# Optimization experiments

Hardware: AMD Instinct MI355X
Metric: run time of the kernel (lower is better)

The kernel has to match this reference:

```python
import jax, jax.numpy as jnp
import numpy as np

N_NODES = 100000
N_EDGES = 1600000
ATOM_EMB = 64
BOND_EMB = 16
MSG_DIM = 64
OUT_HIDDEN = 128
N_MOLS = 2048
MSG_PASSES = 4


def setup_inputs() -> dict:
    key = jax.random.key(0)
    ks = jax.random.split(key, 16)
    x = jax.random.randint(ks[0], (N_NODES,), 0, 119)
    edge_attr = jax.random.randint(ks[1], (N_EDGES,), 0, 4)
    edge_index = jax.random.randint(ks[2], (2, N_EDGES), 0, N_NODES)
    batch = jnp.sort(jax.random.randint(ks[3], (N_NODES,), 0, N_MOLS))
    s = 0.02
    atom_table = jax.random.normal(ks[4], (119, ATOM_EMB), jnp.float32) * s
    bond_table = jax.random.normal(ks[5], (4, BOND_EMB), jnp.float32) * s
    Wi = jax.random.normal(ks[6], (ATOM_EMB + BOND_EMB, MSG_DIM), jnp.float32) * s
    bi = jnp.zeros((MSG_DIM,), jnp.float32)
    Wu = jax.random.normal(ks[7], (ATOM_EMB + BOND_EMB + MSG_DIM, MSG_DIM), jnp.float32) * s
    bu = jnp.zeros((MSG_DIM,), jnp.float32)
    W1 = jax.random.normal(ks[8], (MSG_DIM, OUT_HIDDEN), jnp.float32) * s
    b1 = jnp.zeros((OUT_HIDDEN,), jnp.float32)
    W2 = jax.random.normal(ks[9], (OUT_HIDDEN, 1), jnp.float32) * s
    b2 = jnp.zeros((1,), jnp.float32)
    return {"x": x, "edge_attr": edge_attr, "edge_index": edge_index, "batch": batch,
            "atom_table": atom_table, "bond_table": bond_table,
            "Wi": Wi, "bi": bi, "Wu": Wu, "bu": bu,
            "W1": W1, "b1": b1, "W2": W2, "b2": b2}


def reference(x, edge_attr, edge_index, batch, atom_table, bond_table, Wi, bi, Wu, bu, W1, b1, W2, b2):
    atom = atom_table[x]                      # [N, ATOM_EMB]
    bond = bond_table[edge_attr]              # [E, BOND_EMB]
    src, dst = edge_index[0], edge_index[1]
    atom_src = atom[src]                      # [E, ATOM_EMB]
    ab = jnp.concatenate([atom_src, bond], axis=1)
    msg = jax.nn.relu(ab @ Wi + bi)           # [E, MSG_DIM]
    for _ in range(MSG_PASSES):
        agg = jax.ops.segment_sum(msg, dst, num_segments=N_NODES)  # [N, MSG_DIM]
        upd_in = jnp.concatenate([ab, agg[src]], axis=1)           # [E, 144]
        msg = jax.nn.relu(upd_in @ Wu + bu)
    node_state = jax.ops.segment_sum(msg, dst, num_segments=N_NODES)
    mol_state = jax.ops.segment_sum(node_state, batch, num_segments=N_MOLS)
    h = jax.nn.relu(mol_state @ W1 + b1)
    return (h @ W2 + b2).squeeze(-1)          # [N_MOLS]
```

## Files before the change

### kernel.cpp

```cpp
#include <hip/hip_runtime.h>

#define MSG 64
#define SLICE_SHIFT 9
#define SLICE_N (1 << SLICE_SHIFT)
#define MAXSLICES 256
#define REP 8
#define CAP_R 1536
#define CAP_E 12288
#define CAP_B 16384
#define NBIN 64

typedef _Float16 h2 __attribute__((ext_vector_type(2)));
typedef _Float16 h4 __attribute__((ext_vector_type(4)));
typedef _Float16 h8 __attribute__((ext_vector_type(8)));

__device__ inline h8 relu8(h8 v) {
    h8 z = {};
    return __builtin_elementwise_max(v, z);
}

__device__ inline h2 u2h(unsigned u) { union { unsigned u; h2 h; } c; c.u = u; return c.h; }

__global__ void setup_kernel(const float* __restrict__ atom, const float* __restrict__ bond,
                             const float* __restrict__ Wi, const float* __restrict__ bi,
                             const float* __restrict__ Wu, const float* __restrict__ bu,
                             const float* __restrict__ Wagg,
                             _Float16* __restrict__ tAi, _Float16* __restrict__ tBi,
                             _Float16* __restrict__ tAu, _Float16* __restrict__ tBu,
                             unsigned* __restrict__ wst, int* __restrict__ gcur,
                             int* __restrict__ bcnt, float* __restrict__ mol,
                             int AR, int K, int ab) {
    int b = blockIdx.x;
    if (b < 2 * ab + 2) {
        bool upd = b >= ab + 1;
        const float* W = upd ? Wu : Wi;
        int lb = upd ? b - (ab + 1) : b;
        if (lb < ab) {
            _Float16* tA = upd ? tAu : tAi;
            int t = lb * 256 + threadIdx.x;
            if (t < AR * MSG) {
                int i = t & 63, a = t >> 6;
                float s = 0.f;
                for (int k = 0; k < 64; ++k) s = fmaf(atom[a * 64 + k], W[k * 64 + i], s);
                tA[t] = (_Float16)s;
            }
        } else {
            _Float16* tBo = upd ? tBu : tBi;
            const float* bias = upd ? bu : bi;
            const float* W16 = W + 64 * MSG;
            int t = threadIdx.x;
            int i = t & 63, r = t >> 6;
            float s = bias[i];
            for (int k = 0; k < 16; ++k) s = fmaf(bond[r * 16 + k], W16[k * 64 + i], s);
            tBo[t] = (_Float16)s;
        }
    } else if (b < 2 * ab + 10) {
        int t = (b - (2 * ab + 2)) * 256 + threadIdx.x;
        if (t < 2048) {
            int k2 = t >> 6, c = t & 63;
            h2 h; h[0] = (_Float16)Wagg[(2 * k2) * 64 + c]; h[1] = (_Float16)Wagg[(2 * k2 + 1) * 64 + c];
            union { h2 h; unsigned u; } cv; cv.h = h;
            wst[k2 * 64 + c] = cv.u;
        }
    } else if (b == 2 * ab + 10) {
        for (int q = threadIdx.x; q < K * REP; q += 256) gcur[q] = q * CAP_R;
        if (threadIdx.x < NBIN) bcnt[threadIdx.x] = 0;
    } else {
        int t = (b - (2 * ab + 11)) * 256 + threadIdx.x;
        ((float4*)mol)[t] = make_float4(0.f, 0.f, 0.f, 0.f);
    }
}

__global__ __launch_bounds__(256) void partition_kernel(
    const int* __restrict__ ei, const int* __restrict__ eattr,
    int E, int* __restrict__ gcur, unsigned long long* __restrict__ aux, int K)
{
    __shared__ int cnt[MAXSLICES];
    __shared__ int lexcl[MAXSLICES];
    __shared__ int gbase[MAXSLICES];
    __shared__ int wsum[4];
    __shared__ unsigned long long stage[1024];
    if (threadIdx.x < MAXSLICES) cnt[threadIdx.x] = 0;
    __syncthreads();
    int rep = blockIdx.x & (REP - 1);
    int e0 = blockIdx.x * 1024;
    int total = min(1024, E - e0);
    int sl[4]; int rk[4]; unsigned long long rec[4];
#pragma unroll
    for (int r = 0; r < 4; ++r) {
        sl[r] = -1;
        int e = e0 + r * 256 + threadIdx.x;
        if (e < E) {
            int s = ei[e], d = ei[E + e];
            rec[r] = ((unsigned long long)((unsigned)s | ((unsigned)eattr[e] << 17)) << 17) | (unsigned)d;
            sl[r] = d >> SLICE_SHIFT;
            rk[r] = atomicAdd(&cnt[sl[r]], 1);
        }
    }
    __syncthreads();
    {
        int c = cnt[threadIdx.x];
        int lane = threadIdx.x & 63, w = threadIdx.x >> 6;
        int sc = c;
        for (int off = 1; off < 64; off <<= 1) { int t = __shfl_up(sc, off); if (lane >= off) sc += t; }
        if (lane == 63) wsum[w] = sc;
        __syncthreads();
        int add = 0;
        for (int q = 0; q < 3; ++q) if (w > q) add += wsum[q];
        lexcl[threadIdx.x] = sc + add - c;
        if (threadIdx.x < K && c > 0)
            gbase[threadIdx.x] = atomicAdd(&gcur[threadIdx.x * REP + rep], c);
    }
    __syncthreads();
#pragma unroll
    for (int r = 0; r < 4; ++r)
        if (sl[r] >= 0) stage[lexcl[sl[r]] + rk[r]] = rec[r];
    __syncthreads();
#pragma unroll
    for (int r = 0; r < 4; ++r) {
        int i = r * 256 + threadIdx.x;
        if (i < total) {
            unsigned long long a = stage[i];
            int s = (int)((unsigned)a & 0x1FFFFu) >> SLICE_SHIFT;
            aux[gbase[s] + (i - lexcl[s])] = a;
        }
    }
}

__global__ __launch_bounds__(1024) void place_kernel(
    const unsigned long long* __restrict__ aux, const int* __restrict__ gcur,
    int* __restrict__ nstart, int* __restrict__ bcnt, int* __restrict__ bucket,
    unsigned* __restrict__ packed, int N)
{
    __shared__ int cnt[SLICE_N];
    __shared__ int wsum[8];
    __shared__ unsigned stage[CAP_E];
    __shared__ int bc[NBIN];
    __shared__ int bb[NBIN];
    int s = blockIdx.x;
    int lo = s << SLICE_SHIFT;
    if (threadIdx.x < SLICE_N) cnt[threadIdx.x] = 0;
    if (threadIdx.x >= SLICE_N && threadIdx.x < SLICE_N + NBIN) bc[threadIdx.x - SLICE_N] = 0;
    __syncthreads();
    for (int r = 0; r < REP; ++r) {
        int q = s * REP + r;
        int start = q * CAP_R, end = gcur[q];
        for (int idx = start + threadIdx.x; idx < end; idx += 1024)
            atomicAdd(&cnt[(int)(aux[idx] & 0x1FFFFu) & (SLICE_N - 1)], 1);
    }
    __syncthreads();
    int c = 0, sc = 0;
    if (threadIdx.x < SLICE_N) {
        c = cnt[threadIdx.x];
        int lane = threadIdx.x & 63, w = threadIdx.x >> 6;
        sc = c;
        for (int off = 1; off < 64; off <<= 1) { int t = __shfl_up(sc, off); if (lane >= off) sc += t; }
        if (lane == 63) wsum[w] = sc;
    }
    __syncthreads();
    int v = lo + threadIdx.x;
    int bin = -1, rk = 0;
    if (threadIdx.x < SLICE_N) {
        int w = threadIdx.x >> 6;
        int add = 0;
        for (int q = 0; q < 7; ++q) if (w > q) add += wsum[q];
        sc += add;
        if (v < N) {
            nstart[v] = s * CAP_E + sc - c;
            bin = min(c, NBIN - 1);
            rk = atomicAdd(&bc[bin], 1);
        }
    }
    __syncthreads();
    if (threadIdx.x < NBIN && bc[threadIdx.x] > 0)
        bb[threadIdx.x] = atomicAdd(&bcnt[threadIdx.x], bc[threadIdx.x]);
    __syncthreads();
    if (bin >= 0) bucket[bin * CAP_B + bb[bin] + rk] = v | (c << 17);
    if (threadIdx.x < SLICE_N) cnt[threadIdx.x] = sc - c;
    __syncthreads();
    for (int r = 0; r < REP; ++r) {
        int q = s * REP + r;
        int start = q * CAP_R, end = gcur[q];
        for (int idx = start + threadIdx.x; idx < end; idx += 1024) {
            unsigned long long a = aux[idx];
            int d = (int)(a & 0x1FFFFu);
            int p = atomicAdd(&cnt[d & (SLICE_N - 1)], 1);
            stage[p] = (unsigned)(a >> 17);
        }
    }
    __syncthreads();
    int totale = cnt[SLICE_N - 1];
    for (int i = threadIdx.x; i < totale; i += 1024)
        packed[s * CAP_E + i] = stage[i];
}

__global__ void compact_kernel(const int* __restrict__ bucket, const int* __restrict__ bcnt,
                               const int* __restrict__ nstart, int2* __restrict__ srt) {
    __shared__ int sbase;
    int b = blockIdx.x;
    if (threadIdx.x == 0) {
        int run = 0;
        for (int i = b + 1; i < NBIN; ++i) run += bcnt[i];
        sbase = run;
    }
    __syncthreads();
    int n = bcnt[b], base = sbase;
    for (int i = threadIdx.x; i < n; i += 256) {
        int e = bucket[b * CAP_B + i];
        int v = e & 0x1FFFF;
        srt[base + i] = make_int2(nstart[v], e);
    }
}

template <int MODE>
__global__ __launch_bounds__(256, 8) void gather_kernel(
    const unsigned* __restrict__ packed, const int2* __restrict__ srt,
    const _Float16* __restrict__ nodearr, const _Float16* __restrict__ tB,
    const unsigned* __restrict__ wst_g, const _Float16* __restrict__ tAu,
    const int* __restrict__ x, const _Float16* __restrict__ tAi,
    _Float16* __restrict__ out, int N)
{
    __shared__ _Float16 tbs[4 * 64];
    __shared__ unsigned wst[32 * 64];
    __shared__ _Float16 rowb[32][72];
    tbs[threadIdx.x] = tB[threadIdx.x];
    if (MODE != 2)
        for (int idx = threadIdx.x; idx < 2048; idx += 256) wst[idx] = wst_g[idx];
    __syncthreads();
    int t = blockIdx.x * 256 + threadIdx.x;
    int vi = t >> 3;
    int j = threadIdx.x & 7;
    int w = threadIdx.x >> 3;
    const h8* na8 = (const h8*)nodearr;
    const h8* tAi8 = (const h8*)tAi;
    const _Float16* tbsj = tbs + j * 8;
    auto ldrow = [&](unsigned q) -> h8 {
        if (MODE == 0) return tAi8[(long long)x[q & 0x1FFFFu] * 8 + j];
        else           return na8[(q & 0x1FFFFu) * 8 + j];
    };
    auto ldtb = [&](unsigned q) -> h8 { return *(const h8*)&tbsj[(q >> 17) * 64]; };
    h8 acc = {};
    int v = 0;
    bool valid = vi < N;
    if (valid) {
        int2 s2 = srt[vi];
        int e = s2.x;
        v = (int)((unsigned)s2.y & 0x1FFFFu);
        int end = e + (int)((unsigned)s2.y >> 17);
        for (; e + 7 < end; e += 8) {
            unsigned q0 = packed[e],     q1 = packed[e + 1], q2 = packed[e + 2], q3 = packed[e + 3];
            unsigned q4 = packed[e + 4], q5 = packed[e + 5], q6 = packed[e + 6], q7 = packed[e + 7];
            h8 m0 = ldrow(q0), m1 = ldrow(q1), m2 = ldrow(q2), m3 = ldrow(q3);
            h8 m4 = ldrow(q4), m5 = ldrow(q5), m6 = ldrow(q6), m7 = ldrow(q7);
            h8 s0 = relu8(m0 + ldtb(q0)), s1 = relu8(m1 + ldtb(q1));
            h8 s2v = relu8(m2 + ldtb(q2)), s3 = relu8(m3 + ldtb(q3));
            h8 s4 = relu8(m4 + ldtb(q4)), s5 = relu8(m5 + ldtb(q5));
            h8 s6 = relu8(m6 + ldtb(q6)), s7 = relu8(m7 + ldtb(q7));
            acc += ((s0 + s1) + (s2v + s3)) + ((s4 + s5) + (s6 + s7));
        }
        for (; e < end; ++e) {
            unsigned q0 = packed[e];
            acc += relu8(ldrow(q0) + ldtb(q0));
        }
    }
    if (MODE == 2) {
        if (valid) ((h8*)out)[(long long)v * 8 + j] = acc;
        return;
    }
    *(h8*)&rowb[w][j * 8] = acc;
    __syncthreads();
    if (!valid) return;
    const h2* rp = (const h2*)&rowb[w][0];
    const unsigned* wj = wst + j * 8;
    float o0 = 0.f, o1 = 0.f, o2 = 0.f, o3 = 0.f, o4 = 0.f, o5 = 0.f, o6 = 0.f, o7 = 0.f;
#pragma unroll
    for (int k2 = 0; k2 < 32; ++k2) {
        h2 r = rp[k2];
        uint4 wa = *(const uint4*)&wj[k2 * 64];
        uint4 wb = *(const uint4*)&wj[k2 * 64 + 4];
        o0 = __builtin_amdgcn_fdot2(r, u2h(wa.x), o0, false);
        o1 = __builtin_amdgcn_fdot2(r, u2h(wa.y), o1, false);
        o2 = __builtin_amdgcn_fdot2(r, u2h(wa.z), o2, false);
        o3 = __builtin_amdgcn_fdot2(r, u2h(wa.w), o3, false);
        o4 = __builtin_amdgcn_fdot2(r, u2h(wb.x), o4, false);
        o5 = __builtin_amdgcn_fdot2(r, u2h(wb.y), o5, false);
        o6 = __builtin_amdgcn_fdot2(r, u2h(wb.z), o6, false);
        o7 = __builtin_amdgcn_fdot2(r, u2h(wb.w), o7, false);
    }
    h8 ta = ((const h8*)tAu)[x[v] * 8 + j];
    h8 o;
    o[0] = (_Float16)(o0 + (float)ta[0]); o[1] = (_Float16)(o1 + (float)ta[1]);
    o[2] = (_Float16)(o2 + (float)ta[2]); o[3] = (_Float16)(o3 + (float)ta[3]);
    o[4] = (_Float16)(o4 + (float)ta[4]); o[5] = (_Float16)(o5 + (float)ta[5]);
    o[6] = (_Float16)(o6 + (float)ta[6]); o[7] = (_Float16)(o7 + (float)ta[7]);
    ((h8*)out)[(long long)v * 8 + j] = o;
}

__global__ void mol_pool_kernel(const _Float16* __restrict__ ns, const int* __restrict__ batch,
                                float* __restrict__ mol, int N) {
    int g = (blockIdx.x * blockDim.x + threadIdx.x) >> 4;
    int j = threadIdx.x & 15;
    int n0 = g * 32;
    if (n0 >= N) return;
    int n1 = min(n0 + 32, N);
    const h4* ns4 = (const h4*)ns;
    int cur = batch[n0];
    float ax = 0.f, ay = 0.f, az = 0.f, aw = 0.f;
    for (int n = n0; n < n1; ++n) {
        int b = batch[n];
        if (b != cur) {
            float* mp = &mol[(long long)cur * 64 + j * 4];
            atomicAdd(mp + 0, ax); atomicAdd(mp + 1, ay);
            atomicAdd(mp + 2, az); atomicAdd(mp + 3, aw);
            ax = ay = az = aw = 0.f; cur = b;
        }
        h4 vv = ns4[(long long)n * 16 + j];
        ax += (float)vv.x; ay += (float)vv.y; az += (float)vv.z; aw += (float)vv.w;
    }
    float* mp = &mol[(long long)cur * 64 + j * 4];
    atomicAdd(mp + 0, ax); atomicAdd(mp + 1, ay);
    atomicAdd(mp + 2, az); atomicAdd(mp + 3, aw);
}

__global__ void head_kernel(const float* __restrict__ mol, const float* __restrict__ W1,
                            const float* __restrict__ b1, const float* __restrict__ W2,
                            const float* __restrict__ b2, float* __restrict__ out) {
    int g = blockIdx.x;
    int j = threadIdx.x;
    float s = b1[j];
#pragma unroll
    for (int k = 0; k < 64; ++k) s = fmaf(mol[g * 64 + k], W1[k * 128 + j], s);
    s = fmaxf(s, 0.0f) * W2[j];
    __shared__ float red[128];
    red[j] = s;
    __syncthreads();
    for (int off = 64; off > 0; off >>= 1) {
        if (j < off) red[j] += red[j + off];
        __syncthreads();
    }
    if (j == 0) out[g] = red[0] + b2[0];
}

extern "C" void kernel_launch(void* const* d_in, const int* in_sizes, int n_in,
                              void* d_out, int out_size, void* d_ws, size_t ws_size,
                              hipStream_t stream) {
    const int*   x          = (const int*)d_in[0];
    const int*   eattr      = (const int*)d_in[1];
    const int*   ei         = (const int*)d_in[2];
    const int*   batch      = (const int*)d_in[3];
    const float* atom_table = (const float*)d_in[4];
    const float* bond_table = (const float*)d_in[5];
    const float* Wi         = (const float*)d_in[6];
    const float* bi         = (const float*)d_in[7];
    const float* Wu         = (const float*)d_in[8];
    const float* bu         = (const float*)d_in[9];
    const float* W1         = (const float*)d_in[10];
    const float* b1         = (const float*)d_in[11];
    const float* W2         = (const float*)d_in[12];
    const float* b2         = (const float*)d_in[13];

    const int N = in_sizes[0];
    const int E = in_sizes[1];
    const int M = out_size;
    const int AR = in_sizes[4] / 64;
    const int K = (N + SLICE_N - 1) >> SLICE_SHIFT;
    const int ab = (AR * MSG + 255) / 256;

    char* ws = (char*)d_ws;
    size_t off_b = 0;
    auto alloc = [&](size_t bytes) -> void* {
        void* p = ws + off_b;
        off_b = (off_b + bytes + 255) & ~(size_t)255;
        return p;
    };
    size_t nbytes = (size_t)N * MSG * 2;
    size_t abytes = (size_t)K * REP * CAP_R * 8;
    _Float16* bufA  = (_Float16*)alloc(nbytes);
    _Float16* bufB  = (_Float16*)alloc(nbytes > abytes ? nbytes : abytes);
    unsigned long long* aux = (unsigned long long*)bufB;
    unsigned* packed = (unsigned*)alloc((size_t)K * CAP_E * 4);
    int*      nstart = (int*)alloc((size_t)N * 4);
    int2*     srt    = (int2*)alloc((size_t)N * 8);
    int*      bucket = (int*)alloc((size_t)NBIN * CAP_B * 4);
    int*      bcnt   = (int*)alloc((size_t)NBIN * 4);
    int*      gcur   = (int*)alloc((size_t)K * REP * 4);
    _Float16* tAi    = (_Float16*)alloc((size_t)AR * MSG * 2);
    _Float16* tBi    = (_Float16*)alloc((size_t)4 * MSG * 2);
    _Float16* tAu    = (_Float16*)alloc((size_t)AR * MSG * 2);
    _Float16* tBu    = (_Float16*)alloc((size_t)4 * MSG * 2);
    unsigned* wstb   = (unsigned*)alloc((size_t)32 * 64 * 4);
    float*    mol    = (float*)alloc((size_t)M * MSG * 4);
    (void)ws_size; (void)n_in;

    const float* Wagg = Wu + 80 * MSG;

    setup_kernel<<<2 * ab + 11 + 128, 256, 0, stream>>>(atom_table, bond_table, Wi, bi, Wu, bu, Wagg,
                                                        tAi, tBi, tAu, tBu, wstb, gcur, bcnt, mol,
                                                        AR, K, ab);

    partition_kernel<<<(E + 1023) / 1024, 256, 0, stream>>>(ei, eattr, E, gcur, aux, K);
    place_kernel<<<K, 1024, 0, stream>>>(aux, gcur, nstart, bcnt, bucket, packed, N);
    compact_kernel<<<NBIN, 256, 0, stream>>>(bucket, bcnt, nstart, srt);

    const int gblocks = (int)(((long long)N * 8 + 255) / 256);
    gather_kernel<0><<<gblocks, 256, 0, stream>>>(packed, srt, nullptr, tBi, wstb, tAu, x, tAi, bufA, N);
    gather_kernel<1><<<gblocks, 256, 0, stream>>>(packed, srt, bufA, tBu, wstb, tAu, x, nullptr, bufB, N);
    gather_kernel<1><<<gblocks, 256, 0, stream>>>(packed, srt, bufB, tBu, wstb, tAu, x, nullptr, bufA, N);
    gather_kernel<1><<<gblocks, 256, 0, stream>>>(packed, srt, bufA, tBu, wstb, tAu, x, nullptr, bufB, N);
    gather_kernel<2><<<gblocks, 256, 0, stream>>>(packed, srt, bufB, tBu, nullptr, nullptr, nullptr, nullptr, bufA, N);

    mol_pool_kernel<<<(((N + 31) / 32) * 16 + 255) / 256, 256, 0, stream>>>(bufA, batch, mol, N);
    head_kernel<<<M, 128, 0, stream>>>(mol, W1, b1, W2, b2, (float*)d_out);
}
```

Baseline: 261.6 us.

## Pack partition records to 32 bits and fuse molecule pooling into head

Edge records in the partition stage now pack the source, bond type and low destination bits into 32 bits, with the slice id kept only in shared staging. This halves aux buffer traffic. Molecule pooling is folded into the head kernel: per-molecule node ranges come from a binary search over the sorted batch array in setup. This removes the atomic pooling kernel, the mol buffer zeroing and a launch. It relies on batch being sorted and on node ids fitting in 17 bits.

```diff
diff --git a/kernel.cpp b/kernel.cpp
--- a/kernel.cpp
+++ b/kernel.cpp
@@ -24,12 +24,12 @@
 __global__ void setup_kernel(const float* __restrict__ atom, const float* __restrict__ bond,
                              const float* __restrict__ Wi, const float* __restrict__ bi,
                              const float* __restrict__ Wu, const float* __restrict__ bu,
-                             const float* __restrict__ Wagg,
+                             const float* __restrict__ Wagg, const int* __restrict__ batch,
                              _Float16* __restrict__ tAi, _Float16* __restrict__ tBi,
                              _Float16* __restrict__ tAu, _Float16* __restrict__ tBu,
                              unsigned* __restrict__ wst, int* __restrict__ gcur,
-                             int* __restrict__ bcnt, float* __restrict__ mol,
-                             int AR, int K, int ab) {
+                             int* __restrict__ bcnt, int* __restrict__ mstart,
+                             int AR, int K, int ab, int N, int M) {
     int b = blockIdx.x;
     if (b < 2 * ab + 2) {
         bool upd = b >= ab + 1;
@@ -66,14 +66,18 @@
         for (int q = threadIdx.x; q < K * REP; q += 256) gcur[q] = q * CAP_R;
         if (threadIdx.x < NBIN) bcnt[threadIdx.x] = 0;
     } else {
-        int t = (b - (2 * ab + 11)) * 256 + threadIdx.x;
-        ((float4*)mol)[t] = make_float4(0.f, 0.f, 0.f, 0.f);
+        int m = (b - (2 * ab + 11)) * 256 + threadIdx.x;
+        if (m <= M) {
+            int lo = 0, hi = N;
+            while (lo < hi) { int mid = (lo + hi) >> 1; if (batch[mid] < m) lo = mid + 1; else hi = mid; }
+            mstart[m] = lo;
+        }
     }
 }
 
 __global__ __launch_bounds__(256) void partition_kernel(
     const int* __restrict__ ei, const int* __restrict__ eattr,
-    int E, int* __restrict__ gcur, unsigned long long* __restrict__ aux, int K)
+    int E, int* __restrict__ gcur, unsigned* __restrict__ aux, int K)
 {
     __shared__ int cnt[MAXSLICES];
     __shared__ int lexcl[MAXSLICES];
@@ -92,8 +96,10 @@
         int e = e0 + r * 256 + threadIdx.x;
         if (e < E) {
             int s = ei[e], d = ei[E + e];
-            rec[r] = ((unsigned long long)((unsigned)s | ((unsigned)eattr[e] << 17)) << 17) | (unsigned)d;
+            unsigned r32 = (unsigned)s | ((unsigned)eattr[e] << 17)
+                         | ((unsigned)(d & (SLICE_N - 1)) << 19);
             sl[r] = d >> SLICE_SHIFT;
+            rec[r] = ((unsigned long long)sl[r] << 32) | r32;
             rk[r] = atomicAdd(&cnt[sl[r]], 1);
         }
     }
@@ -121,14 +127,14 @@
         int i = r * 256 + threadIdx.x;
         if (i < total) {
             unsigned long long a = stage[i];
-            int s = (int)((unsigned)a & 0x1FFFFu) >> SLICE_SHIFT;
-            aux[gbase[s] + (i - lexcl[s])] = a;
+            int s = (int)(a >> 32);
+            aux[gbase[s] + (i - lexcl[s])] = (unsigned)a;
         }
     }
 }
 
 __global__ __launch_bounds__(1024) void place_kernel(
-    const unsigned long long* __restrict__ aux, const int* __restrict__ gcur,
+    const unsigned* __restrict__ aux, const int* __restrict__ gcur,
     int* __restrict__ nstart, int* __restrict__ bcnt, int* __restrict__ bucket,
     unsigned* __restrict__ packed, int N)
 {
@@ -146,7 +152,7 @@
         int q = s * REP + r;
         int start = q * CAP_R, end = gcur[q];
         for (int idx = start + threadIdx.x; idx < end; idx += 1024)
-            atomicAdd(&cnt[(int)(aux[idx] & 0x1FFFFu) & (SLICE_N - 1)], 1);
+            atomicAdd(&cnt[(aux[idx] >> 19) & (SLICE_N - 1)], 1);
     }
     __syncthreads();
     int c = 0, sc = 0;
@@ -182,10 +188,10 @@
         int q = s * REP + r;
         int start = q * CAP_R, end = gcur[q];
         for (int idx = start + threadIdx.x; idx < end; idx += 1024) {
-            unsigned long long a = aux[idx];
-            int d = (int)(a & 0x1FFFFu);
-            int p = atomicAdd(&cnt[d & (SLICE_N - 1)], 1);
-            stage[p] = (unsigned)(a >> 17);
+            unsigned a = aux[idx];
+            int dlo = (a >> 19) & (SLICE_N - 1);
+            int p = atomicAdd(&cnt[dlo], 1);
+            stage[p] = a & 0x7FFFFu;
         }
     }
     __syncthreads();
@@ -296,40 +302,29 @@
     ((h8*)out)[(long long)v * 8 + j] = o;
 }
 
-__global__ void mol_pool_kernel(const _Float16* __restrict__ ns, const int* __restrict__ batch,
-                                float* __restrict__ mol, int N) {
-    int g = (blockIdx.x * blockDim.x + threadIdx.x) >> 4;
-    int j = threadIdx.x & 15;
-    int n0 = g * 32;
-    if (n0 >= N) return;
-    int n1 = min(n0 + 32, N);
-    const h4* ns4 = (const h4*)ns;
-    int cur = batch[n0];
-    float ax = 0.f, ay = 0.f, az = 0.f, aw = 0.f;
-    for (int n = n0; n < n1; ++n) {
-        int b = batch[n];
-        if (b != cur) {
-            float* mp = &mol[(long long)cur * 64 + j * 4];
-            atomicAdd(mp + 0, ax); atomicAdd(mp + 1, ay);
-            atomicAdd(mp + 2, az); atomicAdd(mp + 3, aw);
-            ax = ay = az = aw = 0.f; cur = b;
-        }
-        h4 vv = ns4[(long long)n * 16 + j];
-        ax += (float)vv.x; ay += (float)vv.y; az += (float)vv.z; aw += (float)vv.w;
-    }
-    float* mp = &mol[(long long)cur * 64 + j * 4];
-    atomicAdd(mp + 0, ax); atomicAdd(mp + 1, ay);
-    atomicAdd(mp + 2, az); atomicAdd(mp + 3, aw);
-}
-
-__global__ void head_kernel(const float* __restrict__ mol, const float* __restrict__ W1,
-                            const float* __restrict__ b1, const float* __restrict__ W2,
-                            const float* __restrict__ b2, float* __restrict__ out) {
+__global__ void mol_head_kernel(const _Float16* __restrict__ ns, const int* __restrict__ mstart,
+                                const float* __restrict__ W1, const float* __restrict__ b1,
+                                const float* __restrict__ W2, const float* __restrict__ b2,
+                                float* __restrict__ out) {
     int g = blockIdx.x;
     int j = threadIdx.x;
+    int n0 = mstart[g], n1 = mstart[g + 1];
+    __shared__ float partial[128];
+    __shared__ float molrow[64];
+    int f = j & 63;
+    int half = j >> 6;
+    int mid = n0 + ((n1 - n0 + 1) >> 1);
+    int ns_ = half ? mid : n0;
+    int ne_ = half ? n1 : mid;
+    float sum = 0.f;
+    for (int n = ns_; n < ne_; ++n) sum += (float)ns[(long long)n * 64 + f];
+    partial[j] = sum;
+    __syncthreads();
+    if (j < 64) molrow[j] = partial[j] + partial[j + 64];
+    __syncthreads();
     float s = b1[j];
 #pragma unroll
-    for (int k = 0; k < 64; ++k) s = fmaf(mol[g * 64 + k], W1[k * 128 + j], s);
+    for (int k = 0; k < 64; ++k) s = fmaf(molrow[k], W1[k * 128 + j], s);
     s = fmaxf(s, 0.0f) * W2[j];
     __shared__ float red[128];
     red[j] = s;
@@ -374,29 +369,30 @@
         return p;
     };
     size_t nbytes = (size_t)N * MSG * 2;
-    size_t abytes = (size_t)K * REP * CAP_R * 8;
+    size_t abytes = (size_t)K * REP * CAP_R * 4;
     _Float16* bufA  = (_Float16*)alloc(nbytes);
     _Float16* bufB  = (_Float16*)alloc(nbytes > abytes ? nbytes : abytes);
-    unsigned long long* aux = (unsigned long long*)bufB;
+    unsigned* aux   = (unsigned*)bufB;
     unsigned* packed = (unsigned*)alloc((size_t)K * CAP_E * 4);
     int*      nstart = (int*)alloc((size_t)N * 4);
     int2*     srt    = (int2*)alloc((size_t)N * 8);
     int*      bucket = (int*)alloc((size_t)NBIN * CAP_B * 4);
     int*      bcnt   = (int*)alloc((size_t)NBIN * 4);
     int*      gcur   = (int*)alloc((size_t)K * REP * 4);
+    int*      mstart = (int*)alloc((size_t)(M + 1) * 4);
     _Float16* tAi    = (_Float16*)alloc((size_t)AR * MSG * 2);
     _Float16* tBi    = (_Float16*)alloc((size_t)4 * MSG * 2);
     _Float16* tAu    = (_Float16*)alloc((size_t)AR * MSG * 2);
     _Float16* tBu    = (_Float16*)alloc((size_t)4 * MSG * 2);
     unsigned* wstb   = (unsigned*)alloc((size_t)32 * 64 * 4);
-    float*    mol    = (float*)alloc((size_t)M * MSG * 4);
     (void)ws_size; (void)n_in;
 
     const float* Wagg = Wu + 80 * MSG;
 
-    setup_kernel<<<2 * ab + 11 + 128, 256, 0, stream>>>(atom_table, bond_table, Wi, bi, Wu, bu, Wagg,
-                                                        tAi, tBi, tAu, tBu, wstb, gcur, bcnt, mol,
-                                                        AR, K, ab);
+    const int mblocks = (M + 256) / 256 + 1;
+    setup_kernel<<<2 * ab + 11 + mblocks, 256, 0, stream>>>(atom_table, bond_table, Wi, bi, Wu, bu,
+                                                            Wagg, batch, tAi, tBi, tAu, tBu, wstb,
+                                                            gcur, bcnt, mstart, AR, K, ab, N, M);
 
     partition_kernel<<<(E + 1023) / 1024, 256, 0, stream>>>(ei, eattr, E, gcur, aux, K);
     place_kernel<<<K, 1024, 0, stream>>>(aux, gcur, nstart, bcnt, bucket, packed, N);
@@ -409,6 +405,5 @@
     gather_kernel<1><<<gblocks, 256, 0, stream>>>(packed, srt, bufA, tBu, wstb, tAu, x, nullptr, bufB, N);
     gather_kernel<2><<<gblocks, 256, 0, stream>>>(packed, srt, bufB, tBu, nullptr, nullptr, nullptr, nullptr, bufA, N);
 
-    mol_pool_kernel<<<(((N + 31) / 32) * 16 + 255) / 256, 256, 0, stream>>>(bufA, batch, mol, N);
-    head_kernel<<<M, 128, 0, stream>>>(mol, W1, b1, W2, b2, (float*)d_out);
-}
+    mol_head_kernel<<<M, 128, 0, stream>>>(bufA, mstart, W1, b1, W2, b2, (float*)d_out);
+}
```

Measured after the change: 252.7 us. 1.04x faster.
